# Kernel optimization log

Measured on AMD Instinct MI355X. Metric: run time of the kernel, lower is better.

## Reference

```python
import jax, jax.numpy as jnp
import numpy as np

PATCH_SIZE = 50        # hardcoded in forward (overrides __init__ args)
NUM_PATCHES_OUT = 50   # size of the weighted_x buffer
TOPK = 4


def setup_inputs() -> dict:
    key = jax.random.key(0)
    k1, k2 = jax.random.split(key)
    x = jax.random.normal(k1, (1024, 12, 2500), dtype=jnp.float32)
    # self.weights = sigmoid(sample from N(0,1)) -> a scalar in (0,1)
    weights = jax.nn.sigmoid(jax.random.normal(k2, (), dtype=jnp.float32))
    return {"x": x, "weights": weights}


def reference(x, weights):
    B, N, L = x.shape
    # power spectrum |FFT(x)|^2 along time axis
    power = jnp.abs(jnp.fft.fft(x, axis=2)) ** 2            # [B,N,L] f32
    _, idx = jax.lax.top_k(power, TOPK)                      # [B,N,K] descending
    # only lead 0 and topk positions {0, 2} are used by the original code
    idx2 = idx[:, 0, ::2]                                    # [B,2] int32
    # np.fft.fftfreq(L)[i] = i/L for i <= (L-1)//2 else (i-L)/L
    k_signed = jnp.where(idx2 <= (L - 1) // 2, idx2, idx2 - L)
    valid = k_signed != 0                                    # freq == 0 -> skip
    # ideal_peak_interval = int(|1/freq|) = L // |k| (exact integer math)
    period = L // jnp.maximum(jnp.abs(k_signed), 1)          # [B,2] >= 2
    P = L // PATCH_SIZE                                      # effective num_patches
    starts = jnp.arange(P, dtype=jnp.int32) * PATCH_SIZE     # [P]
    # patch [start, start+PATCH_SIZE) contains a peak (multiple of period)
    # iff the first multiple >= start is < start + PATCH_SIZE
    p = period[..., None]                                    # [B,2,1]
    first_mult = ((starts[None, None, :] + p - 1) // p) * p  # [B,2,P]
    hit = (first_mult < starts[None, None, :] + PATCH_SIZE) & valid[..., None]
    counts = hit.sum(axis=1)                                 # [B,P] in {0,1,2}
    # the b/n loops add `weights` N times per (b, patch, freq-slot) hit
    weighted = (N * weights) * counts.astype(jnp.float32)    # [B,P]
    out = jnp.zeros((B, NUM_PATCHES_OUT), jnp.float32).at[:, :P].set(weighted)
    # original detaches via a numpy round-trip -> no gradient flows
    return jax.lax.stop_gradient(out)
```

## Files before the change

kernel.cpp:

```cpp
#include <hip/hip_runtime.h>

typedef _Float16 f16;
typedef _Float16 f16x4 __attribute__((ext_vector_type(4)));
typedef _Float16 f16x8 __attribute__((ext_vector_type(8)));
typedef float f32x4 __attribute__((ext_vector_type(4)));

#define L_N 2500
#define B_N 1024
#define ROWSTRIDE 30000
#define NPATCH 50
#define PATCH 50
#define KP 2560
#define NB 2560
#define ZSPLIT 4
#define KS_PER_Z 20

#define TWOPI_F 6.28318530717958647692f
#define RAD_PER_PH (6.283185307179586476925286766559 / 2500.0)

#define OFF_XH 0
#define SZ_XH (B_N * KP * 2)
#define OFF_W  (OFF_XH + SZ_XH)
#define SZ_W   (NB * KP * 2)
#define OFF_C  (OFF_W + SZ_W)
#define SZ_C   (B_N * NB * 4)

#define PB_X    B_N
#define PB_W    1280
#define PB_Z    (SZ_C / 16 / 256)
#define PB_TOT  (PB_X + PB_W + PB_Z)

#define GLOAD16(gp, lp) __builtin_amdgcn_global_load_lds( \
    (const __attribute__((address_space(1))) unsigned int*)(gp), \
    (__attribute__((address_space(3))) unsigned int*)(lp), 16, 0, 0)

__global__ __launch_bounds__(256)
void prep(const float* __restrict__ x, f16* __restrict__ Xh,
          f16* __restrict__ W, float4* __restrict__ C4) {
    const int b = blockIdx.x, tid = threadIdx.x;
    if (b < PB_X) {
        const int row = b;
#pragma unroll
        for (int i = 0; i < 3; ++i) {
            int slot = tid + 256 * i;
            if (slot < 640) {
                float4 v = make_float4(0.f, 0.f, 0.f, 0.f);
                if (slot < 625)
                    v = *reinterpret_cast<const float4*>(x + (size_t)row * ROWSTRIDE + slot * 4);
                f16x4 h = { (f16)v.x, (f16)v.y, (f16)v.z, (f16)v.w };
                *reinterpret_cast<f16x4*>(Xh + (size_t)row * KP + slot * 4) = h;
            }
        }
    } else if (b < PB_X + PB_W) {
        const int bin = b - PB_X;
        for (int t = tid; t < KP; t += 256) {
            float c = 0.f, s = 0.f;
            if (t < L_N) {
                int ph = (bin * t) % L_N;
                float th = (float)ph * (TWOPI_F / (float)L_N);
                __sincosf(th, &s, &c);
            }
            W[(size_t)(2 * bin) * KP + t]     = (f16)c;
            W[(size_t)(2 * bin + 1) * KP + t] = (f16)s;
        }
    } else {
        int i = (b - PB_X - PB_W) * 256 + tid;
        C4[i] = make_float4(0.f, 0.f, 0.f, 0.f);
    }
}

__global__ __launch_bounds__(256)
void gemm_f16(const f16* __restrict__ A, const f16* __restrict__ W, float* __restrict__ C) {
    __shared__ f16 As[2][128 * 32];
    __shared__ f16 Bs[2][128 * 32];
    const int tid = threadIdx.x;
    const int wv = tid >> 6, lane = tid & 63;
    const int bm = blockIdx.x, bn = blockIdx.y;
    const int ks0 = blockIdx.z * KS_PER_Z;
    const int wr = wv >> 1, wc = wv & 1;
    const int lrow = lane & 15, lseg = lane >> 4;

    f32x4 acc[4][4];
#pragma unroll
    for (int m = 0; m < 4; ++m)
#pragma unroll
        for (int n = 0; n < 4; ++n) acc[m][n] = (f32x4){0.f, 0.f, 0.f, 0.f};

    const int c0 = wv * 128 + lane, c1 = c0 + 64;
    const int R0 = c0 >> 2, S0 = (c0 & 3) ^ ((R0 >> 1) & 3);
    const int R1 = c1 >> 2, S1 = (c1 & 3) ^ ((R1 >> 1) & 3);
    const f16* ga0 = A + (size_t)(bm * 128 + R0) * KP + S0 * 8;
    const f16* ga1 = A + (size_t)(bm * 128 + R1) * KP + S1 * 8;
    const f16* gb0 = W + (size_t)(bn * 128 + R0) * KP + S0 * 8;
    const f16* gb1 = W + (size_t)(bn * 128 + R1) * KP + S1 * 8;

    int aoff[4], boff[4];
#pragma unroll
    for (int m = 0; m < 4; ++m) {
        int ra = wr * 64 + m * 16 + lrow;
        aoff[m] = ra * 32 + ((lseg ^ ((ra >> 1) & 3)) * 8);
        int rb = wc * 64 + m * 16 + lrow;
        boff[m] = rb * 32 + ((lseg ^ ((rb >> 1) & 3)) * 8);
    }

    {
        const int kof = ks0 * 32;
        GLOAD16(ga0 + kof, &As[0][c0 * 8]);
        GLOAD16(ga1 + kof, &As[0][c1 * 8]);
        GLOAD16(gb0 + kof, &Bs[0][c0 * 8]);
        GLOAD16(gb1 + kof, &Bs[0][c1 * 8]);
    }
    __syncthreads();

    int cur = 0;
    for (int t = 0; t < KS_PER_Z; ++t) {
        const int nxt = cur ^ 1;
        if (t + 1 < KS_PER_Z) {
            const int kof = (ks0 + t + 1) * 32;
            GLOAD16(ga0 + kof, &As[nxt][c0 * 8]);
            GLOAD16(ga1 + kof, &As[nxt][c1 * 8]);
            GLOAD16(gb0 + kof, &Bs[nxt][c0 * 8]);
            GLOAD16(gb1 + kof, &Bs[nxt][c1 * 8]);
        }
        f16x8 af[4], bf[4];
#pragma unroll
        for (int m = 0; m < 4; ++m) af[m] = *(const f16x8*)&As[cur][aoff[m]];
#pragma unroll
        for (int n = 0; n < 4; ++n) bf[n] = *(const f16x8*)&Bs[cur][boff[n]];
#pragma unroll
        for (int m = 0; m < 4; ++m)
#pragma unroll
            for (int n = 0; n < 4; ++n)
                acc[m][n] = __builtin_amdgcn_mfma_f32_16x16x32_f16(af[m], bf[n], acc[m][n], 0, 0, 0);
        __syncthreads();
        cur = nxt;
    }

    const int orow0 = bm * 128 + wr * 64 + (lane >> 4) * 4;
    const int ocol0 = bn * 128 + wc * 64 + (lane & 15);
#pragma unroll
    for (int m = 0; m < 4; ++m)
#pragma unroll
        for (int n = 0; n < 4; ++n)
#pragma unroll
            for (int j = 0; j < 4; ++j)
                atomicAdd(&C[(size_t)(orow0 + m * 16 + j) * NB + ocol0 + n * 16], acc[m][n][j]);
}

__global__ __launch_bounds__(512)
void fused_sel(const float* __restrict__ x, const float* __restrict__ C,
               const float* __restrict__ wp, float* __restrict__ out) {
    __shared__ float xrow[KP];
    __shared__ unsigned long long keybuf[64];
    __shared__ int bins8s[8];
    __shared__ unsigned long long rk[8];
    const int row = blockIdx.x, tid = threadIdx.x;
    const int wv = tid >> 6, lane = tid & 63;

    if (tid < 60) xrow[2500 + tid] = 0.f;
#pragma unroll
    for (int i = 0; i < 2; ++i) {
        int slot = tid + 512 * i;
        if (slot < 625)
            *reinterpret_cast<float4*>(&xrow[slot * 4]) =
                *reinterpret_cast<const float4*>(x + (size_t)row * ROWSTRIDE + slot * 4);
    }

    unsigned long long k3[3];
#pragma unroll
    for (int c = 0; c < 3; ++c) {
        int bin = tid + 512 * c;
        unsigned long long key = 0ULL;
        if (bin <= 1250) {
            float2 ri = *reinterpret_cast<const float2*>(&C[(size_t)row * NB + 2 * bin]);
            float p = ri.x * ri.x + ri.y * ri.y;
            key = ((unsigned long long)__float_as_uint(p) << 32) | (unsigned)(L_N - bin);
        }
        k3[c] = key;
    }
#pragma unroll
    for (int r = 0; r < 8; ++r) {
        unsigned long long m = k3[0];
        m = (k3[1] > m) ? k3[1] : m;
        m = (k3[2] > m) ? k3[2] : m;
#pragma unroll
        for (int off = 32; off > 0; off >>= 1) {
            unsigned long long o = __shfl_xor(m, off, 64);
            m = (o > m) ? o : m;
        }
        if (k3[0] == m) k3[0] = 0ULL;
        if (k3[1] == m) k3[1] = 0ULL;
        if (k3[2] == m) k3[2] = 0ULL;
        if (lane == 0) keybuf[wv * 8 + r] = m;
    }
    __syncthreads();
    if (wv == 0) {
        unsigned long long cur = keybuf[lane];
#pragma unroll
        for (int r = 0; r < 8; ++r) {
            unsigned long long m = cur;
#pragma unroll
            for (int off = 32; off > 0; off >>= 1) {
                unsigned long long o = __shfl_xor(m, off, 64);
                m = (o > m) ? o : m;
            }
            if (cur == m) cur = 0ULL;
            if (lane == 0) bins8s[r] = L_N - (int)(unsigned)(m & 0xffffffffULL);
        }
    }
    __syncthreads();

    const int k = bins8s[wv];
    double c, s, cd, sd;
    {
        int ph0 = (k * lane) % L_N;
        int phd = (k * 64) % L_N;
        sincos((double)ph0 * RAD_PER_PH, &s, &c);
        sincos((double)phd * RAD_PER_PH, &sd, &cd);
    }
    double re = 0.0, im = 0.0;
#pragma unroll 4
    for (int i = 0; i < 40; ++i) {
        double xv = (double)xrow[lane + 64 * i];
        re += xv * c;
        im += xv * s;
        double cn = c * cd - s * sd;
        double sn = s * cd + c * sd;
        c = cn; s = sn;
    }
#pragma unroll
    for (int off = 32; off > 0; off >>= 1) {
        re += __shfl_xor(re, off, 64);
        im += __shfl_xor(im, off, 64);
    }
    if (lane == 0) {
        double p = re * re + im * im;
        unsigned long long pb = (unsigned long long)__double_as_longlong(p);
        rk[wv] = (pb & ~2047ULL) | (unsigned long long)(1250 - k);
    }
    __syncthreads();

    if (tid < NPATCH) {
        unsigned long long q[8];
#pragma unroll
        for (int r = 0; r < 8; ++r) q[r] = rk[r];
        unsigned long long m1 = q[0];
#pragma unroll
        for (int r = 1; r < 8; ++r) m1 = (q[r] > m1) ? q[r] : m1;
#pragma unroll
        for (int r = 0; r < 8; ++r) if (q[r] == m1) q[r] = 0;
        unsigned long long m2 = q[0];
#pragma unroll
        for (int r = 1; r < 8; ++r) m2 = (q[r] > m2) ? q[r] : m2;
#pragma unroll
        for (int r = 0; r < 8; ++r) if (q[r] == m2) q[r] = 0;
        unsigned long long m3 = q[0];
#pragma unroll
        for (int r = 1; r < 8; ++r) m3 = (q[r] > m3) ? q[r] : m3;

        int kA = 1250 - (int)(m1 & 2047ULL);
        int kB = 1250 - (int)(m2 & 2047ULL);
        int kC = 1250 - (int)(m3 & 2047ULL);
        int multA = (kA == 0 || kA == 1250) ? 1 : 2;
        int multB = (kB == 0 || kB == 1250) ? 1 : 2;
        int sel0 = kA;
        int sel1 = (multA == 2 || multB == 2) ? kB : kC;

        int start = tid * PATCH;
        int cnt = 0;
        if (sel0 != 0) {
            int p = L_N / sel0;
            int fm = ((start + p - 1) / p) * p;
            if (fm < start + PATCH) ++cnt;
        }
        if (sel1 != 0) {
            int p = L_N / sel1;
            int fm = ((start + p - 1) / p) * p;
            if (fm < start + PATCH) ++cnt;
        }
        out[(size_t)row * NPATCH + tid] = 12.0f * wp[0] * (float)cnt;
    }
}

extern "C" void kernel_launch(void* const* d_in, const int* in_sizes, int n_in,
                              void* d_out, int out_size, void* d_ws, size_t ws_size,
                              hipStream_t stream) {
    const float* x = (const float*)d_in[0];
    const float* w = (const float*)d_in[1];
    float* out = (float*)d_out;
    char* ws = (char*)d_ws;

    f16* Xh = (f16*)(ws + OFF_XH);
    f16* W  = (f16*)(ws + OFF_W);
    float* C = (float*)(ws + OFF_C);

    prep<<<PB_TOT, 256, 0, stream>>>(x, Xh, W, (float4*)C);
    gemm_f16<<<dim3(8, 20, ZSPLIT), 256, 0, stream>>>(Xh, W, C);
    fused_sel<<<B_N, 512, 0, stream>>>(x, C, w, out);
}
```

Before: 228.5 us.

## Double GEMM K-tile depth to 64 with 8-way swizzle; vectorize twiddle writes

After: 229.1 us. Within noise of the previous version (+0.3%).

```diff
diff --git a/kernel.cpp b/kernel.cpp
--- a/kernel.cpp
+++ b/kernel.cpp
@@ -1,6 +1,7 @@
 #include <hip/hip_runtime.h>
 
 typedef _Float16 f16;
+typedef _Float16 f16x2 __attribute__((ext_vector_type(2)));
 typedef _Float16 f16x4 __attribute__((ext_vector_type(4)));
 typedef _Float16 f16x8 __attribute__((ext_vector_type(8)));
 typedef float f32x4 __attribute__((ext_vector_type(4)));
@@ -13,7 +14,7 @@
 #define KP 2560
 #define NB 2560
 #define ZSPLIT 4
-#define KS_PER_Z 20
+#define KS_PER_Z 10
 
 #define TWOPI_F 6.28318530717958647692f
 #define RAD_PER_PH (6.283185307179586476925286766559 / 2500.0)
@@ -53,15 +54,25 @@
         }
     } else if (b < PB_X + PB_W) {
         const int bin = b - PB_X;
-        for (int t = tid; t < KP; t += 256) {
-            float c = 0.f, s = 0.f;
+#pragma unroll
+        for (int i = 0; i < 5; ++i) {
+            int t2 = tid + 256 * i;
+            int t = 2 * t2;
+            float c0 = 0.f, s0 = 0.f, c1 = 0.f, s1 = 0.f;
             if (t < L_N) {
                 int ph = (bin * t) % L_N;
                 float th = (float)ph * (TWOPI_F / (float)L_N);
-                __sincosf(th, &s, &c);
-            }
-            W[(size_t)(2 * bin) * KP + t]     = (f16)c;
-            W[(size_t)(2 * bin + 1) * KP + t] = (f16)s;
+                __sincosf(th, &s0, &c0);
+            }
+            if (t + 1 < L_N) {
+                int ph = (bin * (t + 1)) % L_N;
+                float th = (float)ph * (TWOPI_F / (float)L_N);
+                __sincosf(th, &s1, &c1);
+            }
+            f16x2 cc = { (f16)c0, (f16)c1 };
+            f16x2 ss = { (f16)s0, (f16)s1 };
+            *reinterpret_cast<f16x2*>(&W[(size_t)(2 * bin) * KP + t])     = cc;
+            *reinterpret_cast<f16x2*>(&W[(size_t)(2 * bin + 1) * KP + t]) = ss;
         }
     } else {
         int i = (b - PB_X - PB_W) * 256 + tid;
@@ -71,8 +82,8 @@
 
 __global__ __launch_bounds__(256)
 void gemm_f16(const f16* __restrict__ A, const f16* __restrict__ W, float* __restrict__ C) {
-    __shared__ f16 As[2][128 * 32];
-    __shared__ f16 Bs[2][128 * 32];
+    __shared__ f16 As[2][128 * 64];
+    __shared__ f16 Bs[2][128 * 64];
     const int tid = threadIdx.x;
     const int wv = tid >> 6, lane = tid & 63;
     const int bm = blockIdx.x, bn = blockIdx.y;
@@ -86,29 +97,36 @@
 #pragma unroll
         for (int n = 0; n < 4; ++n) acc[m][n] = (f32x4){0.f, 0.f, 0.f, 0.f};
 
-    const int c0 = wv * 128 + lane, c1 = c0 + 64;
-    const int R0 = c0 >> 2, S0 = (c0 & 3) ^ ((R0 >> 1) & 3);
-    const int R1 = c1 >> 2, S1 = (c1 & 3) ^ ((R1 >> 1) & 3);
-    const f16* ga0 = A + (size_t)(bm * 128 + R0) * KP + S0 * 8;
-    const f16* ga1 = A + (size_t)(bm * 128 + R1) * KP + S1 * 8;
-    const f16* gb0 = W + (size_t)(bn * 128 + R0) * KP + S0 * 8;
-    const f16* gb1 = W + (size_t)(bn * 128 + R1) * KP + S1 * 8;
-
-    int aoff[4], boff[4];
+    const f16* ga[4];
+    const f16* gb[4];
+    int ldst[4];
+#pragma unroll
+    for (int i = 0; i < 4; ++i) {
+        int c = tid + 256 * i;
+        int R = c >> 3, S = (c & 7) ^ (R & 7);
+        ga[i] = A + (size_t)(bm * 128 + R) * KP + S * 8;
+        gb[i] = W + (size_t)(bn * 128 + R) * KP + S * 8;
+        ldst[i] = c * 8;
+    }
+
+    int aoff[4][2], boff[4][2];
 #pragma unroll
     for (int m = 0; m < 4; ++m) {
-        int ra = wr * 64 + m * 16 + lrow;
-        aoff[m] = ra * 32 + ((lseg ^ ((ra >> 1) & 3)) * 8);
-        int rb = wc * 64 + m * 16 + lrow;
-        boff[m] = rb * 32 + ((lseg ^ ((rb >> 1) & 3)) * 8);
-    }
-
-    {
-        const int kof = ks0 * 32;
-        GLOAD16(ga0 + kof, &As[0][c0 * 8]);
-        GLOAD16(ga1 + kof, &As[0][c1 * 8]);
-        GLOAD16(gb0 + kof, &Bs[0][c0 * 8]);
-        GLOAD16(gb1 + kof, &Bs[0][c1 * 8]);
+#pragma unroll
+        for (int kh = 0; kh < 2; ++kh) {
+            int ra = wr * 64 + m * 16 + lrow;
+            int sa = (lseg + kh * 4) ^ (ra & 7);
+            aoff[m][kh] = ra * 64 + sa * 8;
+            int rb = wc * 64 + m * 16 + lrow;
+            int sb = (lseg + kh * 4) ^ (rb & 7);
+            boff[m][kh] = rb * 64 + sb * 8;
+        }
+    }
+
+#pragma unroll
+    for (int i = 0; i < 4; ++i) {
+        GLOAD16(ga[i] + ks0 * 64, &As[0][ldst[i]]);
+        GLOAD16(gb[i] + ks0 * 64, &Bs[0][ldst[i]]);
     }
     __syncthreads();
 
@@ -116,22 +134,26 @@
     for (int t = 0; t < KS_PER_Z; ++t) {
         const int nxt = cur ^ 1;
         if (t + 1 < KS_PER_Z) {
-            const int kof = (ks0 + t + 1) * 32;
-            GLOAD16(ga0 + kof, &As[nxt][c0 * 8]);
-            GLOAD16(ga1 + kof, &As[nxt][c1 * 8]);
-            GLOAD16(gb0 + kof, &Bs[nxt][c0 * 8]);
-            GLOAD16(gb1 + kof, &Bs[nxt][c1 * 8]);
-        }
-        f16x8 af[4], bf[4];
-#pragma unroll
-        for (int m = 0; m < 4; ++m) af[m] = *(const f16x8*)&As[cur][aoff[m]];
-#pragma unroll
-        for (int n = 0; n < 4; ++n) bf[n] = *(const f16x8*)&Bs[cur][boff[n]];
-#pragma unroll
-        for (int m = 0; m < 4; ++m)
-#pragma unroll
-            for (int n = 0; n < 4; ++n)
-                acc[m][n] = __builtin_amdgcn_mfma_f32_16x16x32_f16(af[m], bf[n], acc[m][n], 0, 0, 0);
+            const int kof = (ks0 + t + 1) * 64;
+#pragma unroll
+            for (int i = 0; i < 4; ++i) {
+                GLOAD16(ga[i] + kof, &As[nxt][ldst[i]]);
+                GLOAD16(gb[i] + kof, &Bs[nxt][ldst[i]]);
+            }
+        }
+#pragma unroll
+        for (int kh = 0; kh < 2; ++kh) {
+            f16x8 af[4], bf[4];
+#pragma unroll
+            for (int m = 0; m < 4; ++m) af[m] = *(const f16x8*)&As[cur][aoff[m][kh]];
+#pragma unroll
+            for (int n = 0; n < 4; ++n) bf[n] = *(const f16x8*)&Bs[cur][boff[n][kh]];
+#pragma unroll
+            for (int m = 0; m < 4; ++m)
+#pragma unroll
+                for (int n = 0; n < 4; ++n)
+                    acc[m][n] = __builtin_amdgcn_mfma_f32_16x16x32_f16(af[m], bf[n], acc[m][n], 0, 0, 0);
+        }
         __syncthreads();
         cur = nxt;
     }
```
